# Kernel tuning notes

Hardware: AMD Instinct MI355X
Metric: run time of the kernel (lower is better)

Reference implementation:

```python
import jax, jax.numpy as jnp
import numpy as np

B, T, C = 4, 2048, 2048
D_ATT, D_FFN = 2048, 8192
EPS = 1e-5

def setup_inputs() -> dict:
    key = jax.random.key(0)
    ks = jax.random.split(key, 20)
    n = lambda k, s, sc=0.02: jax.random.normal(k, s, dtype=jnp.float32) * sc
    u = lambda k, s: jax.random.uniform(k, s, dtype=jnp.float32)
    return {
        'x': jax.random.normal(ks[0], (B, T, C), dtype=jnp.float32),
        'ln1_w': jnp.ones((C,), jnp.float32), 'ln1_b': jnp.zeros((C,), jnp.float32),
        'ln2_w': jnp.ones((C,), jnp.float32), 'ln2_b': jnp.zeros((C,), jnp.float32),
        'tm_k': u(ks[1], (1, 1, C)), 'tm_v': u(ks[2], (1, 1, C)), 'tm_r': u(ks[3], (1, 1, C)),
        'time_decay': n(ks[4], (D_ATT,), 1.0),            # raw; decay = -exp(time_decay)
        'time_first': n(ks[5], (D_ATT,), 0.3) + float(np.log(0.3)),
        'Wk': n(ks[6], (D_ATT, C)), 'Wv': n(ks[7], (D_ATT, C)),
        'Wr': n(ks[8], (D_ATT, C)), 'Wo': n(ks[9], (C, D_ATT)),
        'cm_k': u(ks[10], (1, 1, C)), 'cm_r': u(ks[11], (1, 1, C)),
        'Wck': n(ks[12], (D_FFN, C)), 'Wcv': n(ks[13], (C, D_FFN)), 'Wcr': n(ks[14], (C, C)),
    }

def layer_norm(x, w, b):
    mu = jnp.mean(x, axis=-1, keepdims=True)
    var = jnp.var(x, axis=-1, keepdims=True)
    return (x - mu) * jax.lax.rsqrt(var + EPS) * w + b

def time_shift(x):
    # xx[:, t] = x[:, t-1], zero at t=0
    return jnp.pad(x, ((0, 0), (1, 0), (0, 0)))[:, :-1]

def wkv(time_decay, time_first, k, v):
    # Numerically-stable WKV linear recurrence (RWKV-4). k, v: [B,T,D]
    decay = -jnp.exp(time_decay)  # [D]
    kT = jnp.swapaxes(k, 0, 1)    # [T,B,D]
    vT = jnp.swapaxes(v, 0, 1)

    def step(carry, kv_t):
        aa, bb, pp = carry
        kt, vt = kv_t
        ww = time_first + kt
        p = jnp.maximum(pp, ww)
        e1 = jnp.exp(pp - p)
        e2 = jnp.exp(ww - p)
        out = (e1 * aa + e2 * vt) / (e1 * bb + e2)
        ww2 = pp + decay
        p2 = jnp.maximum(ww2, kt)
        e1b = jnp.exp(ww2 - p2)
        e2b = jnp.exp(kt - p2)
        return (e1b * aa + e2b * vt, e1b * bb + e2b, p2), out

    z = jnp.zeros((k.shape[0], k.shape[2]), k.dtype)
    init = (z, z, jnp.full_like(z, -1e38))
    _, outT = jax.lax.scan(step, init, (kT, vT))
    return jnp.swapaxes(outT, 0, 1)  # [B,T,D]

def reference(x, ln1_w, ln1_b, ln2_w, ln2_b, tm_k, tm_v, tm_r,
              time_decay, time_first, Wk, Wv, Wr, Wo,
              cm_k, cm_r, Wck, Wcv, Wcr):
    # --- TimeMix ---
    h = layer_norm(x, ln1_w, ln1_b)
    hh = time_shift(h)
    xk = h * tm_k + hh * (1 - tm_k)
    xv = h * tm_v + hh * (1 - tm_v)
    xr = h * tm_r + hh * (1 - tm_r)
    k = jnp.einsum('btc,dc->btd', xk, Wk)
    v = jnp.einsum('btc,dc->btd', xv, Wv)
    sr = jax.nn.sigmoid(jnp.einsum('btc,dc->btd', xr, Wr))
    rwkv = sr * wkv(time_decay, time_first, k, v)
    x = x + jnp.einsum('btd,cd->btc', rwkv, Wo)
    # --- ChannelMix ---
    g = layer_norm(x, ln2_w, ln2_b)
    gg = time_shift(g)
    xk2 = g * cm_k + gg * (1 - cm_k)
    xr2 = g * cm_r + gg * (1 - cm_r)
    kf = jnp.square(jax.nn.relu(jnp.einsum('btc,fc->btf', xk2, Wck)))
    kv = jnp.einsum('btf,cf->btc', kf, Wcv)
    x = x + jax.nn.sigmoid(jnp.einsum('btc,dc->btd', xr2, Wcr)) * kv
    return x
```

## Files before the change

kernel.cpp:

```cpp
#include <hip/hip_runtime.h>
#include <hip/hip_bf16.h>

#define B_ 4
#define T_ 2048
#define C_ 2048
#define D_ 2048
#define F_ 8192
#define BT_ (B_*T_)
#define NCH 64
#define LCH 32

using bf16 = __hip_bfloat16;
typedef __attribute__((ext_vector_type(8))) short bf16x8;
typedef __attribute__((ext_vector_type(4))) float f32x4;

struct bf4 { bf16 a, b, c, d; };

__device__ __forceinline__ bf4 to_bf4(float x, float y, float z, float w) {
  bf4 r;
  r.a = __float2bfloat16(x); r.b = __float2bfloat16(y);
  r.c = __float2bfloat16(z); r.d = __float2bfloat16(w);
  return r;
}

__global__ __launch_bounds__(256) void cvt_kernel(const float* __restrict__ in,
                                                  bf16* __restrict__ out, int n4) {
  int i = blockIdx.x * blockDim.x + threadIdx.x;
  int stride = gridDim.x * blockDim.x;
  for (; i < n4; i += stride) {
    float4 v = ((const float4*)in)[i];
    ((bf4*)out)[i] = to_bf4(v.x, v.y, v.z, v.w);
  }
}

__global__ __launch_bounds__(256) void packcvt_kernel(const float* __restrict__ in,
    bf16* __restrict__ out, int rows, int cols_out, int ld_in, int col0) {
  int n4 = rows * (cols_out >> 2);
  int c4 = cols_out >> 2;
  int i = blockIdx.x * blockDim.x + threadIdx.x;
  int stride = gridDim.x * blockDim.x;
  for (; i < n4; i += stride) {
    int r = i / c4;
    int j4 = i - r * c4;
    float4 v = *(const float4*)(in + (size_t)r * ld_in + col0 + j4 * 4);
    ((bf4*)out)[i] = to_bf4(v.x, v.y, v.z, v.w);
  }
}

__device__ __forceinline__ void block_reduce4(float v[4], float out[4]) {
  #pragma unroll
  for (int i = 0; i < 4; ++i)
    #pragma unroll
    for (int off = 1; off < 64; off <<= 1)
      v[i] += __shfl_xor(v[i], off);
  __shared__ float red[4][4];
  int wave = threadIdx.x >> 6, lane = threadIdx.x & 63;
  if (lane == 0) {
    red[wave][0] = v[0]; red[wave][1] = v[1];
    red[wave][2] = v[2]; red[wave][3] = v[3];
  }
  __syncthreads();
  #pragma unroll
  for (int i = 0; i < 4; ++i)
    out[i] = red[0][i] + red[1][i] + red[2][i] + red[3][i];
}

__global__ __launch_bounds__(256) void mix1f_kernel(const float* __restrict__ x,
    const float* __restrict__ w, const float* __restrict__ b,
    const float* __restrict__ tmk, const float* __restrict__ tmv, const float* __restrict__ tmr,
    bf16* __restrict__ xk, bf16* __restrict__ xv, bf16* __restrict__ xr) {
  const int row = blockIdx.x;
  const int t = row & (T_ - 1);
  const bool hasPrev = (t != 0);
  const int tid = threadIdx.x;
  const float* xc = x + (size_t)row * C_;
  const float* xp = xc - C_;
  float c[8], p[8];
  *(float4*)&c[0] = *(const float4*)(xc + tid * 4);
  *(float4*)&c[4] = *(const float4*)(xc + tid * 4 + 1024);
  if (hasPrev) {
    *(float4*)&p[0] = *(const float4*)(xp + tid * 4);
    *(float4*)&p[4] = *(const float4*)(xp + tid * 4 + 1024);
  } else {
    #pragma unroll
    for (int j = 0; j < 8; ++j) p[j] = 0.f;
  }
  float v[4] = {0.f, 0.f, 0.f, 0.f}, tot[4];
  #pragma unroll
  for (int j = 0; j < 8; ++j) {
    v[0] += c[j]; v[1] += c[j] * c[j];
    v[2] += p[j]; v[3] += p[j] * p[j];
  }
  block_reduce4(v, tot);
  const float muc = tot[0] * (1.f / C_);
  const float rsc = rsqrtf(tot[1] * (1.f / C_) - muc * muc + 1e-5f);
  const float mup = tot[2] * (1.f / C_);
  const float rsp = rsqrtf(tot[3] * (1.f / C_) - mup * mup + 1e-5f);
  float wv[8], bv[8], mk[8], mv[8], mr[8];
  #pragma unroll
  for (int half = 0; half < 2; ++half) {
    int i = tid * 4 + half * 1024;
    *(float4*)&wv[half*4] = *(const float4*)(w + i);
    *(float4*)&bv[half*4] = *(const float4*)(b + i);
    *(float4*)&mk[half*4] = *(const float4*)(tmk + i);
    *(float4*)&mv[half*4] = *(const float4*)(tmv + i);
    *(float4*)&mr[half*4] = *(const float4*)(tmr + i);
  }
  float ok[8], ov[8], orr[8];
  #pragma unroll
  for (int j = 0; j < 8; ++j) {
    float h  = (c[j] - muc) * rsc * wv[j] + bv[j];
    float hh = hasPrev ? ((p[j] - mup) * rsp * wv[j] + bv[j]) : 0.f;
    ok[j]  = hh + mk[j] * (h - hh);
    ov[j]  = hh + mv[j] * (h - hh);
    orr[j] = hh + mr[j] * (h - hh);
  }
  size_t ro = (size_t)row * C_;
  #pragma unroll
  for (int half = 0; half < 2; ++half) {
    int i = tid * 4 + half * 1024;
    *(bf4*)(xk + ro + i) = to_bf4(ok[half*4], ok[half*4+1], ok[half*4+2], ok[half*4+3]);
    *(bf4*)(xv + ro + i) = to_bf4(ov[half*4], ov[half*4+1], ov[half*4+2], ov[half*4+3]);
    *(bf4*)(xr + ro + i) = to_bf4(orr[half*4], orr[half*4+1], orr[half*4+2], orr[half*4+3]);
  }
}

__global__ __launch_bounds__(256) void mix2f_kernel(const float* __restrict__ x,
    const float* __restrict__ w, const float* __restrict__ b,
    const float* __restrict__ cmk, const float* __restrict__ cmr,
    bf16* __restrict__ xk2, bf16* __restrict__ xr2) {
  const int row = blockIdx.x;
  const int t = row & (T_ - 1);
  const bool hasPrev = (t != 0);
  const int tid = threadIdx.x;
  const float* xc = x + (size_t)row * C_;
  const float* xp = xc - C_;
  float c[8], p[8];
  *(float4*)&c[0] = *(const float4*)(xc + tid * 4);
  *(float4*)&c[4] = *(const float4*)(xc + tid * 4 + 1024);
  if (hasPrev) {
    *(float4*)&p[0] = *(const float4*)(xp + tid * 4);
    *(float4*)&p[4] = *(const float4*)(xp + tid * 4 + 1024);
  } else {
    #pragma unroll
    for (int j = 0; j < 8; ++j) p[j] = 0.f;
  }
  float v[4] = {0.f, 0.f, 0.f, 0.f}, tot[4];
  #pragma unroll
  for (int j = 0; j < 8; ++j) {
    v[0] += c[j]; v[1] += c[j] * c[j];
    v[2] += p[j]; v[3] += p[j] * p[j];
  }
  block_reduce4(v, tot);
  const float muc = tot[0] * (1.f / C_);
  const float rsc = rsqrtf(tot[1] * (1.f / C_) - muc * muc + 1e-5f);
  const float mup = tot[2] * (1.f / C_);
  const float rsp = rsqrtf(tot[3] * (1.f / C_) - mup * mup + 1e-5f);
  float wv[8], bv[8], mk[8], mr[8];
  #pragma unroll
  for (int half = 0; half < 2; ++half) {
    int i = tid * 4 + half * 1024;
    *(float4*)&wv[half*4] = *(const float4*)(w + i);
    *(float4*)&bv[half*4] = *(const float4*)(b + i);
    *(float4*)&mk[half*4] = *(const float4*)(cmk + i);
    *(float4*)&mr[half*4] = *(const float4*)(cmr + i);
  }
  float ok[8], orr[8];
  #pragma unroll
  for (int j = 0; j < 8; ++j) {
    float h  = (c[j] - muc) * rsc * wv[j] + bv[j];
    float hh = hasPrev ? ((p[j] - mup) * rsp * wv[j] + bv[j]) : 0.f;
    ok[j]  = hh + mk[j] * (h - hh);
    orr[j] = hh + mr[j] * (h - hh);
  }
  size_t ro = (size_t)row * C_;
  #pragma unroll
  for (int half = 0; half < 2; ++half) {
    int i = tid * 4 + half * 1024;
    *(bf4*)(xk2 + ro + i) = to_bf4(ok[half*4], ok[half*4+1], ok[half*4+2], ok[half*4+3]);
    *(bf4*)(xr2 + ro + i) = to_bf4(orr[half*4], orr[half*4+1], orr[half*4+2], orr[half*4+3]);
  }
}

__global__ __launch_bounds__(256) void wkv_pass1(
    const bf16* __restrict__ kp, const bf16* __restrict__ vp,
    const float* __restrict__ td,
    float* __restrict__ sA, float* __restrict__ sB, float* __restrict__ sP) {
  const int g = blockIdx.x * 256 + threadIdx.x;
  const int d = g & (D_ - 1);
  const int c = (g >> 11) & (NCH - 1);
  const int b = g >> 17;
  const float w = -__expf(td[d]);
  const size_t base = ((size_t)b * T_ + c * LCH) * D_ + d;
  float aa = 0.f, bb = 0.f, pp = -1e38f;
  #pragma unroll 4
  for (int j = 0; j < LCH; ++j) {
    float kt = __bfloat162float(kp[base + (size_t)j * D_]);
    float vt = __bfloat162float(vp[base + (size_t)j * D_]);
    float ww2 = pp + w;
    float p2 = fmaxf(ww2, kt);
    float e1 = __expf(ww2 - p2), e2 = __expf(kt - p2);
    aa = e1 * aa + e2 * vt;
    bb = e1 * bb + e2;
    pp = p2;
  }
  const int sidx = ((b * NCH + c) << 11) + d;
  sA[sidx] = aa; sB[sidx] = bb; sP[sidx] = pp;
}

__global__ __launch_bounds__(256) void wkv_pass2(
    const float* __restrict__ td,
    float* __restrict__ sA, float* __restrict__ sB, float* __restrict__ sP) {
  const int g = blockIdx.x * 256 + threadIdx.x;
  const int d = g & (D_ - 1);
  const int b = g >> 11;
  const float wL = -__expf(td[d]) * (float)LCH;
  float aa = 0.f, bb = 0.f, pp = -1e38f;
  for (int c = 0; c < NCH; ++c) {
    const int sidx = ((b * NCH + c) << 11) + d;
    float la = sA[sidx], lb = sB[sidx], lp = sP[sidx];
    sA[sidx] = aa; sB[sidx] = bb; sP[sidx] = pp;
    float ww2 = pp + wL;
    float q = fmaxf(ww2, lp);
    float e1 = __expf(ww2 - q), e2 = __expf(lp - q);
    aa = e1 * aa + e2 * la;
    bb = e1 * bb + e2 * lb;
    pp = q;
  }
}

__global__ __launch_bounds__(256) void wkv_pass3(
    const bf16* __restrict__ kp, const bf16* __restrict__ vp, const bf16* __restrict__ rp,
    const float* __restrict__ td, const float* __restrict__ tfp,
    const float* __restrict__ sA, const float* __restrict__ sB, const float* __restrict__ sP,
    bf16* __restrict__ rwkv) {
  const int g = blockIdx.x * 256 + threadIdx.x;
  const int d = g & (D_ - 1);
  const int c = (g >> 11) & (NCH - 1);
  const int b = g >> 17;
  const float w = -__expf(td[d]);
  const float u = tfp[d];
  const int sidx = ((b * NCH + c) << 11) + d;
  float aa = sA[sidx], bb = sB[sidx], pp = sP[sidx];
  const size_t base = ((size_t)b * T_ + c * LCH) * D_ + d;
  #pragma unroll 4
  for (int j = 0; j < LCH; ++j) {
    float kt = __bfloat162float(kp[base + (size_t)j * D_]);
    float vt = __bfloat162float(vp[base + (size_t)j * D_]);
    float rt = __bfloat162float(rp[base + (size_t)j * D_]);
    float ww = u + kt;
    float p = fmaxf(pp, ww);
    float e1 = __expf(pp - p);
    float e2 = __expf(ww - p);
    float outv = (e1 * aa + e2 * vt) / (e1 * bb + e2);
    float sr = 1.f / (1.f + __expf(-rt));
    rwkv[base + (size_t)j * D_] = __float2bfloat16(sr * outv);
    float ww2 = pp + w;
    float p2 = fmaxf(ww2, kt);
    float e1b = __expf(ww2 - p2);
    float e2b = __expf(kt - p2);
    aa = e1b * aa + e2b * vt;
    bb = e1b * bb + e2b;
    pp = p2;
  }
}

template<int EPI>
__global__ __launch_bounds__(512, 2) void gemm256(
    const bf16* __restrict__ A, const bf16* __restrict__ Bt,
    int N, int K,
    float* __restrict__ outF, bf16* __restrict__ outB,
    const float* __restrict__ addP, const bf16* __restrict__ sigP) {
  __shared__ alignas(16) char lds[131072];
  const int tid = threadIdx.x;
  const int wid = tid >> 6, lane = tid & 63;
  const int wm = wid >> 2, wn = wid & 3;

  const int nwg = gridDim.x;
  const int id = blockIdx.x;
  const int cpx = nwg >> 3;
  const int sid = (id & 7) * cpx + (id >> 3);
  const int nx = N >> 8;
  const int by = sid / nx, bx = sid - by * nx;
  const int tileM = by * 256, tileN = bx * 256;

  const int NT = K >> 6;

  const int srow_lo = wid * 8 + (lane >> 3);
  const int scel = ((lane & 7) ^ (lane >> 3)) << 3;

  const bf16* pA[2][2];
  const bf16* pB[2][2];
  #pragma unroll
  for (int h = 0; h < 2; ++h)
    #pragma unroll
    for (int j = 0; j < 2; ++j) {
      pA[h][j] = A  + (size_t)(tileM + h * 128 + srow_lo + j * 64) * K + scel;
      pB[h][j] = Bt + (size_t)(tileN + h * 128 + srow_lo + j * 64) * K + scel;
    }
  const int ldsW = wid * 1024;

  auto stA = [&](int par, int h) {
    #pragma unroll
    for (int j = 0; j < 2; ++j) {
      __builtin_amdgcn_global_load_lds(
          (const __attribute__((address_space(1))) void*)pA[h][j],
          (__attribute__((address_space(3))) void*)(lds + par * 32768 + h * 16384 + j * 8192 + ldsW),
          16, 0, 0);
      pA[h][j] += 64;
    }
  };
  auto stB = [&](int par, int h) {
    #pragma unroll
    for (int j = 0; j < 2; ++j) {
      __builtin_amdgcn_global_load_lds(
          (const __attribute__((address_space(1))) void*)pB[h][j],
          (__attribute__((address_space(3))) void*)(lds + 65536 + par * 32768 + h * 16384 + j * 8192 + ldsW),
          16, 0, 0);
      pB[h][j] += 64;
    }
  };

  const int lane15 = lane & 15;
  const int kswz0 = ((lane >> 4) * 16) ^ ((lane & 7) << 4);
  const int aBase = (wm * 128 + lane15) * 128;
  const int bBase = (wn * 64 + lane15) * 128;

  f32x4 acc[8][4] = {};

  stB(0, 0); stB(0, 1); stA(0, 0); stA(0, 1);
  if (NT > 1) { stB(1, 0); stB(1, 1); }
  asm volatile("s_waitcnt vmcnt(4)" : : : "memory");
  __builtin_amdgcn_s_barrier();
  __builtin_amdgcn_sched_barrier(0);

  for (int t = 0; t < NT; ++t) {
    const char* Ab = lds + ((t & 1) << 15);
    const char* Bb = lds + 65536 + ((t & 1) << 15);
    const int parA = (t + 1) & 1;
    const int parB = t & 1;
    const bool doA = (t + 1 < NT), doB = (t + 2 < NT);
    bf16x8 bfr[4][2];
    #pragma unroll
    for (int q = 0; q < 4; ++q) {
      if (q == 0) {
        #pragma unroll
        for (int n = 0; n < 4; ++n) {
          bfr[n][0] = *(const bf16x8*)(Bb + bBase + n * 2048 + kswz0);
          bfr[n][1] = *(const bf16x8*)(Bb + bBase + n * 2048 + (kswz0 ^ 64));
        }
      }
      bf16x8 am[2][2];
      #pragma unroll
      for (int mm = 0; mm < 2; ++mm) {
        am[mm][0] = *(const bf16x8*)(Ab + aBase + q * 4096 + mm * 2048 + kswz0);
        am[mm][1] = *(const bf16x8*)(Ab + aBase + q * 4096 + mm * 2048 + (kswz0 ^ 64));
      }
      __builtin_amdgcn_sched_barrier(0);
      if (q == 0 && doA) stA(parA, 0);
      if (q == 1) { if (doA) stA(parA, 1); if (doB) stB(parB, 0); }
      if (q == 2 && doB) stB(parB, 1);
      __builtin_amdgcn_sched_barrier(0);
      __builtin_amdgcn_s_barrier();
      __builtin_amdgcn_sched_barrier(0);
      __builtin_amdgcn_s_setprio(1);
      #pragma unroll
      for (int kk = 0; kk < 2; ++kk)
        #pragma unroll
        for (int n = 0; n < 4; ++n) {
          acc[2*q+0][n] = __builtin_amdgcn_mfma_f32_16x16x32_bf16(am[0][kk], bfr[n][kk], acc[2*q+0][n], 0, 0, 0);
          acc[2*q+1][n] = __builtin_amdgcn_mfma_f32_16x16x32_bf16(am[1][kk], bfr[n][kk], acc[2*q+1][n], 0, 0, 0);
        }
      __builtin_amdgcn_s_setprio(0);
      __builtin_amdgcn_sched_barrier(0);
      if (q == 3 && t + 1 < NT) {
        if (t + 2 < NT) asm volatile("s_waitcnt vmcnt(4)" : : : "memory");
        else            asm volatile("s_waitcnt vmcnt(0)" : : : "memory");
      }
      __builtin_amdgcn_s_barrier();
      __builtin_amdgcn_sched_barrier(0);
    }
  }

  const int erow0 = tileM + wm * 128 + (lane >> 4) * 4;
  const int ecol0 = tileN + wn * 64 + lane15;
  #pragma unroll
  for (int m = 0; m < 8; ++m) {
    #pragma unroll
    for (int n = 0; n < 4; ++n) {
      #pragma unroll
      for (int r = 0; r < 4; ++r) {
        const int grow = erow0 + m * 16 + r;
        const int gcol = ecol0 + n * 16;
        const size_t idx = (size_t)grow * N + gcol;
        const float val = acc[m][n][r];
        if constexpr (EPI == 0) {
          outB[idx] = __float2bfloat16(val);
        } else if constexpr (EPI == 1) {
          float tt = fmaxf(val, 0.f);
          outB[idx] = __float2bfloat16(tt * tt);
        } else if constexpr (EPI == 2) {
          outF[idx] = addP[idx] + val;
        } else if constexpr (EPI == 3) {
          outB[idx] = __float2bfloat16(1.f / (1.f + __expf(-val)));
        } else {
          outF[idx] = addP[idx] + __bfloat162float(sigP[idx]) * val;
        }
      }
    }
  }
}

extern "C" void kernel_launch(void* const* d_in, const int* in_sizes, int n_in,
                              void* d_out, int out_size, void* d_ws, size_t ws_size,
                              hipStream_t stream) {
  const float* x    = (const float*)d_in[0];
  const float* ln1w = (const float*)d_in[1];
  const float* ln1b = (const float*)d_in[2];
  const float* ln2w = (const float*)d_in[3];
  const float* ln2b = (const float*)d_in[4];
  const float* tmk  = (const float*)d_in[5];
  const float* tmv  = (const float*)d_in[6];
  const float* tmr  = (const float*)d_in[7];
  const float* td   = (const float*)d_in[8];
  const float* tf   = (const float*)d_in[9];
  const float* Wk   = (const float*)d_in[10];
  const float* Wv   = (const float*)d_in[11];
  const float* Wr   = (const float*)d_in[12];
  const float* Wo   = (const float*)d_in[13];
  const float* cmk  = (const float*)d_in[14];
  const float* cmr  = (const float*)d_in[15];
  const float* Wck  = (const float*)d_in[16];
  const float* Wcv  = (const float*)d_in[17];
  const float* Wcr  = (const float*)d_in[18];
  float* out = (float*)d_out;

  char* ws = (char*)d_ws;
  const size_t MB = 1ull << 20;
  bf16* R0 = (bf16*)(ws + 0 * MB);
  bf16* R1 = (bf16*)(ws + 32 * MB);
  bf16* R2 = (bf16*)(ws + 64 * MB);
  bf16* R3 = (bf16*)(ws + 96 * MB);
  bf16* R4 = (bf16*)(ws + 128 * MB);

  int S = (ws_size >= 256 * MB) ? 1 : (ws_size >= 192 * MB ? 2 : 4);
  const int FS = F_ / S;

  bf16* xk = R1, *xv = R2, *xr = R3;
  bf16* k_ = R4, *v_ = R1, *r_ = R2, *rwkv = R3;
  bf16* xk2 = R1, *xr2 = R2, *sig = R3, *kf = R4;

  float* sA = (float*)R0;
  float* sB = sA + (size_t)B_ * NCH * D_;
  float* sP = sB + (size_t)B_ * NCH * D_;

  const int gN2k = (BT_ / 256) * (D_ / 256);

  mix1f_kernel<<<BT_, 256, 0, stream>>>(x, ln1w, ln1b, tmk, tmv, tmr, xk, xv, xr);
  cvt_kernel<<<1024, 256, 0, stream>>>(Wk, R0, D_ * C_ / 4);
  gemm256<0><<<gN2k, 512, 0, stream>>>(xk, R0, D_, C_, nullptr, k_, nullptr, nullptr);
  cvt_kernel<<<1024, 256, 0, stream>>>(Wv, R0, D_ * C_ / 4);
  gemm256<0><<<gN2k, 512, 0, stream>>>(xv, R0, D_, C_, nullptr, v_, nullptr, nullptr);
  cvt_kernel<<<1024, 256, 0, stream>>>(Wr, R0, D_ * C_ / 4);
  gemm256<0><<<gN2k, 512, 0, stream>>>(xr, R0, D_, C_, nullptr, r_, nullptr, nullptr);
  wkv_pass1<<<B_ * NCH * D_ / 256, 256, 0, stream>>>(k_, v_, td, sA, sB, sP);
  wkv_pass2<<<B_ * D_ / 256, 256, 0, stream>>>(td, sA, sB, sP);
  wkv_pass3<<<B_ * NCH * D_ / 256, 256, 0, stream>>>(k_, v_, r_, td, tf, sA, sB, sP, rwkv);
  cvt_kernel<<<1024, 256, 0, stream>>>(Wo, R0, C_ * D_ / 4);
  gemm256<2><<<gN2k, 512, 0, stream>>>(rwkv, R0, C_, D_, out, nullptr, x, nullptr);

  mix2f_kernel<<<BT_, 256, 0, stream>>>(out, ln2w, ln2b, cmk, cmr, xk2, xr2);
  cvt_kernel<<<1024, 256, 0, stream>>>(Wcr, R0, C_ * C_ / 4);
  gemm256<3><<<gN2k, 512, 0, stream>>>(xr2, R0, C_, C_, nullptr, sig, nullptr, nullptr);
  for (int h = 0; h < S; ++h) {
    cvt_kernel<<<1024, 256, 0, stream>>>(Wck + (size_t)h * FS * C_, R0, FS * C_ / 4);
    gemm256<1><<<(BT_/256) * (FS/256), 512, 0, stream>>>(xk2, R0, FS, C_, nullptr, kf, nullptr, nullptr);
    packcvt_kernel<<<1024, 256, 0, stream>>>(Wcv, R0, C_, FS, F_, h * FS);
    gemm256<4><<<gN2k, 512, 0, stream>>>(kf, R0, C_, FS, out, nullptr, out, sig);
  }
}
```

Measured before the change: 1.009 ms.

## Switch GEMM inner loop to 32x32x16 MFMA and peel pipeline tail iterations

The GEMM main loop now uses 32x32x16 bf16 MFMA instructions instead of 16x16x32. The LDS fragment addressing, the swizzle and the epilogue row/column mapping are rewritten to match the larger output tile per instruction. Each wave now issues fewer, larger MFMAs with fewer fragment loads per flop. The K-loop is also templated so the last two iterations are peeled, removing the per-iteration prefetch branches. Risks include a different register/accumulator layout and the hard assumption that NT >= 2.

```diff
diff --git a/kernel.cpp b/kernel.cpp
--- a/kernel.cpp
+++ b/kernel.cpp
@@ -13,6 +13,9 @@
 using bf16 = __hip_bfloat16;
 typedef __attribute__((ext_vector_type(8))) short bf16x8;
 typedef __attribute__((ext_vector_type(4))) float f32x4;
+typedef __attribute__((ext_vector_type(16))) float f32x16;
+
+template<bool V> struct BC { static constexpr bool value = V; };
 
 struct bf4 { bf16 a, b, c, d; };
 
@@ -321,79 +324,87 @@
     }
   };
 
-  const int lane15 = lane & 15;
-  const int kswz0 = ((lane >> 4) * 16) ^ ((lane & 7) << 4);
-  const int aBase = (wm * 128 + lane15) * 128;
-  const int bBase = (wn * 64 + lane15) * 128;
-
-  f32x4 acc[8][4] = {};
-
-  stB(0, 0); stB(0, 1); stA(0, 0); stA(0, 1);
-  if (NT > 1) { stB(1, 0); stB(1, 1); }
+  const int lane31 = lane & 31;
+  const int L = lane & 7;
+  int kb[4];
+  #pragma unroll
+  for (int ks = 0; ks < 4; ++ks)
+    kb[ks] = ((((ks << 1) | (lane >> 5)) ^ L) << 4);
+  const int aBase = (wm * 128 + lane31) * 128;
+  const int bBase = (wn * 64 + lane31) * 128;
+
+  f32x16 acc[4][2] = {};
+
+  stB(0, 0); stB(0, 1); stA(0, 0); stA(0, 1); stB(1, 0); stB(1, 1);
   asm volatile("s_waitcnt vmcnt(4)" : : : "memory");
   __builtin_amdgcn_s_barrier();
   __builtin_amdgcn_sched_barrier(0);
 
-  for (int t = 0; t < NT; ++t) {
+  auto tileBody = [&](int t, auto doa, auto dob) {
+    constexpr bool DOA = decltype(doa)::value;
+    constexpr bool DOB = decltype(dob)::value;
     const char* Ab = lds + ((t & 1) << 15);
     const char* Bb = lds + 65536 + ((t & 1) << 15);
     const int parA = (t + 1) & 1;
     const int parB = t & 1;
-    const bool doA = (t + 1 < NT), doB = (t + 2 < NT);
-    bf16x8 bfr[4][2];
+    bf16x8 bfr[2][4];
     #pragma unroll
     for (int q = 0; q < 4; ++q) {
       if (q == 0) {
         #pragma unroll
-        for (int n = 0; n < 4; ++n) {
-          bfr[n][0] = *(const bf16x8*)(Bb + bBase + n * 2048 + kswz0);
-          bfr[n][1] = *(const bf16x8*)(Bb + bBase + n * 2048 + (kswz0 ^ 64));
-        }
-      }
-      bf16x8 am[2][2];
+        for (int n = 0; n < 2; ++n)
+          #pragma unroll
+          for (int ks = 0; ks < 4; ++ks)
+            bfr[n][ks] = *(const bf16x8*)(Bb + bBase + n * 4096 + kb[ks]);
+      }
+      bf16x8 am[4];
       #pragma unroll
-      for (int mm = 0; mm < 2; ++mm) {
-        am[mm][0] = *(const bf16x8*)(Ab + aBase + q * 4096 + mm * 2048 + kswz0);
-        am[mm][1] = *(const bf16x8*)(Ab + aBase + q * 4096 + mm * 2048 + (kswz0 ^ 64));
-      }
+      for (int ks = 0; ks < 4; ++ks)
+        am[ks] = *(const bf16x8*)(Ab + aBase + q * 4096 + kb[ks]);
       __builtin_amdgcn_sched_barrier(0);
-      if (q == 0 && doA) stA(parA, 0);
-      if (q == 1) { if (doA) stA(parA, 1); if (doB) stB(parB, 0); }
-      if (q == 2 && doB) stB(parB, 1);
+      if constexpr (DOA) {
+        if (q == 0) stA(parA, 0);
+        if (q == 1) stA(parA, 1);
+      }
+      if constexpr (DOB) {
+        if (q == 1) stB(parB, 0);
+        if (q == 2) stB(parB, 1);
+      }
       __builtin_amdgcn_sched_barrier(0);
       __builtin_amdgcn_s_barrier();
       __builtin_amdgcn_sched_barrier(0);
       __builtin_amdgcn_s_setprio(1);
       #pragma unroll
-      for (int kk = 0; kk < 2; ++kk)
-        #pragma unroll
-        for (int n = 0; n < 4; ++n) {
-          acc[2*q+0][n] = __builtin_amdgcn_mfma_f32_16x16x32_bf16(am[0][kk], bfr[n][kk], acc[2*q+0][n], 0, 0, 0);
-          acc[2*q+1][n] = __builtin_amdgcn_mfma_f32_16x16x32_bf16(am[1][kk], bfr[n][kk], acc[2*q+1][n], 0, 0, 0);
-        }
+      for (int ks = 0; ks < 4; ++ks) {
+        acc[q][0] = __builtin_amdgcn_mfma_f32_32x32x16_bf16(am[ks], bfr[0][ks], acc[q][0], 0, 0, 0);
+        acc[q][1] = __builtin_amdgcn_mfma_f32_32x32x16_bf16(am[ks], bfr[1][ks], acc[q][1], 0, 0, 0);
+      }
       __builtin_amdgcn_s_setprio(0);
       __builtin_amdgcn_sched_barrier(0);
-      if (q == 3 && t + 1 < NT) {
-        if (t + 2 < NT) asm volatile("s_waitcnt vmcnt(4)" : : : "memory");
-        else            asm volatile("s_waitcnt vmcnt(0)" : : : "memory");
+      if (q == 3) {
+        if constexpr (DOB)      asm volatile("s_waitcnt vmcnt(4)" : : : "memory");
+        else if constexpr (DOA) asm volatile("s_waitcnt vmcnt(0)" : : : "memory");
       }
       __builtin_amdgcn_s_barrier();
       __builtin_amdgcn_sched_barrier(0);
     }
-  }
-
-  const int erow0 = tileM + wm * 128 + (lane >> 4) * 4;
-  const int ecol0 = tileN + wn * 64 + lane15;
-  #pragma unroll
-  for (int m = 0; m < 8; ++m) {
-    #pragma unroll
-    for (int n = 0; n < 4; ++n) {
+  };
+
+  for (int t = 0; t < NT - 2; ++t) tileBody(t, BC<true>{}, BC<true>{});
+  tileBody(NT - 2, BC<true>{}, BC<false>{});
+  tileBody(NT - 1, BC<false>{}, BC<false>{});
+
+  const int h5 = (lane >> 5) * 4;
+  #pragma unroll
+  for (int m = 0; m < 4; ++m) {
+    #pragma unroll
+    for (int n = 0; n < 2; ++n) {
       #pragma unroll
-      for (int r = 0; r < 4; ++r) {
-        const int grow = erow0 + m * 16 + r;
-        const int gcol = ecol0 + n * 16;
+      for (int reg = 0; reg < 16; ++reg) {
+        const int grow = tileM + wm * 128 + m * 32 + (reg & 3) + 8 * (reg >> 2) + h5;
+        const int gcol = tileN + wn * 64 + n * 32 + lane31;
         const size_t idx = (size_t)grow * N + gcol;
-        const float val = acc[m][n][r];
+        const float val = acc[m][n][reg];
         if constexpr (EPI == 0) {
           outB[idx] = __float2bfloat16(val);
         } else if constexpr (EPI == 1) {
```

Measured after the change: 1.078 ms. +6.8%, slower.
